# Kernel optimization log

Hardware: AMD Instinct MI355X
Metric: run time of the kernel (lower is better)

## Reference

```python
import jax, jax.numpy as jnp
import numpy as np

D = 1  # dilation


def _unfold3x3(x, d):
    # x: [B, C, H, W] -> [B, H*W, 9, C]; matches torch.nn.Unfold(kernel_size=3,
    # dilation=d, padding=d, stride=1) followed by the module's reshapes.
    B, C, H, W = x.shape
    xp = jnp.pad(x, ((0, 0), (0, 0), (d, d), (d, d)))
    pats = [xp[:, :, i * d:i * d + H, j * d:j * d + W] for i in range(3) for j in range(3)]
    p = jnp.stack(pats, axis=0)  # [9, B, C, H, W], kernel positions row-major (center = 4)
    return p.transpose(1, 3, 4, 0, 2).reshape(B, H * W, 9, C)


def _masked_bn(h, m, gamma, beta, eps=1e-5):
    # BatchNorm1d in training mode applied only to rows selected by bool mask m
    # (the torch code gathers rows, BNs them, scatters back into zeros).
    # Stats are the biased mean/var over the selected rows, per channel.
    axes = tuple(range(h.ndim - 1))
    mf = m[..., None].astype(h.dtype)
    n = jnp.maximum(mf.sum(), 1.0)
    mean = (h * mf).sum(axes) / n
    var = (((h - mean) ** 2 * mf)).sum(axes) / n
    return (h - mean) * jax.lax.rsqrt(var + eps) * gamma + beta


def setup_inputs() -> dict:
    key = jax.random.key(0)
    ks = jax.random.split(key, 8)
    B, H, W = 2, 64, 1024
    Cin, Cout, Cm = 64, 64, 4
    s = 0.1
    x = jax.random.normal(ks[0], (B, Cm + Cin, H, W), jnp.float32)
    mask = (jax.random.uniform(ks[1], (B, 1, H, W)) > 0.3).astype(jnp.float32)
    return {
        "x": x,
        "mask": mask,
        "w1": jax.random.normal(ks[2], (8, Cm), jnp.float32) * s,
        "bn1_g": jnp.ones(8, jnp.float32),
        "bn1_b": jnp.zeros(8, jnp.float32),
        "w2": jax.random.normal(ks[3], (1, 8), jnp.float32) * s,
        "b2": jnp.zeros(1, jnp.float32),
        "g1": jax.random.normal(ks[4], (8, Cm), jnp.float32) * s,
        "gbn1_g": jnp.ones(8, jnp.float32),
        "gbn1_b": jnp.zeros(8, jnp.float32),
        "g2": jax.random.normal(ks[5], (8, 8), jnp.float32) * s,
        "gbn2_g": jnp.ones(8, jnp.float32),
        "gbn2_b": jnp.zeros(8, jnp.float32),
        "w_agg": jax.random.normal(ks[6], (Cout, 72 + Cin), jnp.float32) * s,
        "abn_g": jnp.ones(Cout, jnp.float32),
        "abn_b": jnp.zeros(Cout, jnp.float32),
    }


def reference(x, mask, w1, bn1_g, bn1_b, w2, b2, g1, gbn1_g, gbn1_b, g2, gbn2_g, gbn2_b, w_agg, abn_g, abn_b):
    B, C, H, W = x.shape
    xu = _unfold3x3(x, D)                      # [B, HW, 9, C]
    mu = _unfold3x3(mask, D)[..., 0]           # [B, HW, 9]
    msel = mu > 0                              # valid-neighbor mask
    mp0 = msel[:, :, 4]                        # valid-center mask [B, HW]
    pn = xu[..., :4] - xu[:, :, 4:5, :4]       # relative meta coords [B, HW, 9, 4]
    feats = xu[..., 4:]                        # neighbor features [B, HW, 9, Cin]

    # weight branch (dense compute + mask == torch's gather/scatter)
    h = _masked_bn(pn @ w1.T, msel, bn1_g, bn1_b)
    h = jax.nn.relu(h) @ w2.T + b2             # [B, HW, 9, 1]
    wts = jnp.where(msel, h[..., 0], 0.0)      # zeros at invalid neighbors pre-softmax
    wts = jax.nn.softmax(wts, axis=-1)[..., None]

    fagg = (wts * feats).sum(axis=2)           # [B, HW, Cin]

    # geo branch
    g = jax.nn.relu(_masked_bn(pn @ g1.T, msel, gbn1_g, gbn1_b))
    g = jax.nn.relu(_masked_bn(g @ g2.T, msel, gbn2_g, gbn2_b))
    g = jnp.where(msel[..., None], g, 0.0)
    g = (wts * g).reshape(B, H * W, 72)

    # aggregation over valid centers
    out = jnp.concatenate([fagg, g], axis=-1) @ w_agg.T
    out = jax.nn.relu(_masked_bn(out, mp0, abn_g, abn_b))
    out = jnp.where(mp0[..., None], out, 0.0)  # [B, HW, Cout]
    return out.transpose(0, 2, 1).reshape(B, -1, H, W)  # fold with k=1 == reshape
```

## Files before the change

kernel.cpp:

```cpp
#include <hip/hip_runtime.h>

#define HW_ 65536
#define W_ 1024
#define H_ 64
#define B_ 2
#define C_ 68
#define NPIX 131072
#define EPS 1e-5f
#define SCOLS 258
#define STOT (15 * SCOLS)

typedef __attribute__((ext_vector_type(8))) short short8;
typedef __attribute__((ext_vector_type(4))) float floatx4;

__device__ __forceinline__ unsigned short f2bf(float f) {
  unsigned u = __float_as_uint(f);
  u += 0x7fffu + ((u >> 16) & 1u);
  return (unsigned short)(u >> 16);
}
__device__ __forceinline__ unsigned pack2(float a, float b) {
  return (unsigned)f2bf(a) | ((unsigned)f2bf(b) << 16);
}
__device__ __forceinline__ float wred(float v) {
  v += __shfl_xor(v, 1);  v += __shfl_xor(v, 2);  v += __shfl_xor(v, 4);
  v += __shfl_xor(v, 8);  v += __shfl_xor(v, 16); v += __shfl_xor(v, 32);
  return v;
}
__device__ __forceinline__ int swz_tile(int bid) {
  return (bid & 7) * 64 + (bid >> 3);
}

#define XSTG(ch, row, col) stg[((ch) * 3 + (row)) * SCOLS + (col)]
#define MSTG(row, col)     stg[(12 + (row)) * SCOLS + (col)]

template <int NT>
__device__ __forceinline__ void stage_rows(const float* xb, const float* mb,
                                           int h, int w0, float* stg, int tid) {
#pragma unroll 1
  for (int i = tid; i < STOT; i += NT) {
    int seg = i / SCOLS, col = i - seg * SCOLS;
    int arr = seg / 3, row = seg - arr * 3;
    int wg = w0 - 1 + col, hg = h + row - 1;
    bool ok = ((unsigned)wg < (unsigned)W_) && ((unsigned)hg < (unsigned)H_);
    float v = 0.f;
    if (ok) v = (arr < 4) ? xb[(size_t)arr * HW_ + (hg << 10) + wg]
                          : mb[(hg << 10) + wg];
    stg[i] = v;
  }
}

__global__ __launch_bounds__(256, 4) void k_stats1(
    const float* __restrict__ x, const float* __restrict__ mask,
    const float* __restrict__ w1, const float* __restrict__ g1,
    float* __restrict__ ws) {
  __shared__ float stg[STOT];
  __shared__ float red[4][34];
  int half = blockIdx.x >> 9;
  int tile = swz_tile(blockIdx.x & 511);
  int p0 = tile * 256;
  int b = p0 >> 16, s0 = p0 & (HW_ - 1);
  int h = s0 >> 10, w0 = s0 & (W_ - 1);
  const float* xb = x + (size_t)b * C_ * HW_;
  const float* mb = mask + (size_t)b * HW_;
  stage_rows<256>(xb, mb, h, w0, stg, threadIdx.x);
  __syncthreads();

  int pix = threadIdx.x;
  float xc0 = XSTG(0, 1, 1 + pix), xc1 = XSTG(1, 1, 1 + pix);
  float xc2 = XSTG(2, 1, 1 + pix), xc3 = XSTG(3, 1, 1 + pix);

  float acc[34];
#pragma unroll
  for (int i = 0; i < 34; i++) acc[i] = 0.f;
  if (half == 0) acc[33] = (MSTG(1, 1 + pix) > 0.f) ? 1.f : 0.f;

  int kb = half ? 5 : 0, ke = half ? 9 : 5;
#pragma unroll
  for (int k = 0; k < 9; k++) {
    if (k < kb || k >= ke) continue;
    int row = k / 3, col = 1 + pix + (k % 3 - 1);
    float mval = MSTG(row, col);
    if (mval > 0.f) {
      float pn0 = XSTG(0, row, col) - xc0;
      float pn1 = XSTG(1, row, col) - xc1;
      float pn2 = XSTG(2, row, col) - xc2;
      float pn3 = XSTG(3, row, col) - xc3;
      acc[32] += 1.f;
#pragma unroll
      for (int o = 0; o < 8; o++) {
        float ta = pn0 * w1[o * 4] + pn1 * w1[o * 4 + 1] + pn2 * w1[o * 4 + 2] + pn3 * w1[o * 4 + 3];
        acc[o] += ta; acc[8 + o] += ta * ta;
        float tg = pn0 * g1[o * 4] + pn1 * g1[o * 4 + 1] + pn2 * g1[o * 4 + 2] + pn3 * g1[o * 4 + 3];
        acc[16 + o] += tg; acc[24 + o] += tg * tg;
      }
    }
  }
  int lane = threadIdx.x & 63, wave = threadIdx.x >> 6;
#pragma unroll
  for (int i = 0; i < 34; i++) {
    float rv = wred(acc[i]);
    if (lane == 0) red[wave][i] = rv;
  }
  __syncthreads();
  if (threadIdx.x < 34)
    atomicAdd(&ws[threadIdx.x],
              red[0][threadIdx.x] + red[1][threadIdx.x] + red[2][threadIdx.x] + red[3][threadIdx.x]);
}

__global__ __launch_bounds__(256, 4) void k_stats2(
    const float* __restrict__ x, const float* __restrict__ mask,
    const float* __restrict__ g1, const float* __restrict__ gbn1_g,
    const float* __restrict__ gbn1_b, const float* __restrict__ g2,
    float* __restrict__ ws) {
  __shared__ float stg[STOT];
  __shared__ float red[4][16];
  __shared__ float sc[8], sh[8];
  if (threadIdx.x < 8) {
    int o = threadIdx.x;
    float n = fmaxf(ws[32], 1.f);
    float mean = ws[16 + o] / n;
    float var = ws[24 + o] / n - mean * mean;
    float s_ = gbn1_g[o] * rsqrtf(var + EPS);
    sc[o] = s_; sh[o] = gbn1_b[o] - mean * s_;
  }
  int half = blockIdx.x >> 9;
  int tile = swz_tile(blockIdx.x & 511);
  int p0 = tile * 256;
  int b = p0 >> 16, s0 = p0 & (HW_ - 1);
  int h = s0 >> 10, w0 = s0 & (W_ - 1);
  const float* xb = x + (size_t)b * C_ * HW_;
  const float* mb = mask + (size_t)b * HW_;
  stage_rows<256>(xb, mb, h, w0, stg, threadIdx.x);
  __syncthreads();

  int pix = threadIdx.x;
  float xc0 = XSTG(0, 1, 1 + pix), xc1 = XSTG(1, 1, 1 + pix);
  float xc2 = XSTG(2, 1, 1 + pix), xc3 = XSTG(3, 1, 1 + pix);

  float acc2[16];
#pragma unroll
  for (int i = 0; i < 16; i++) acc2[i] = 0.f;

  int kb = half ? 5 : 0, ke = half ? 9 : 5;
#pragma unroll
  for (int k = 0; k < 9; k++) {
    if (k < kb || k >= ke) continue;
    int row = k / 3, col = 1 + pix + (k % 3 - 1);
    float mval = MSTG(row, col);
    if (mval > 0.f) {
      float pn0 = XSTG(0, row, col) - xc0;
      float pn1 = XSTG(1, row, col) - xc1;
      float pn2 = XSTG(2, row, col) - xc2;
      float pn3 = XSTG(3, row, col) - xc3;
      float gb[8];
#pragma unroll
      for (int o = 0; o < 8; o++) {
        float tg = pn0 * g1[o * 4] + pn1 * g1[o * 4 + 1] + pn2 * g1[o * 4 + 2] + pn3 * g1[o * 4 + 3];
        gb[o] = fmaxf(sc[o] * tg + sh[o], 0.f);
      }
#pragma unroll
      for (int j = 0; j < 8; j++) {
        float t2 = 0.f;
#pragma unroll
        for (int o = 0; o < 8; o++) t2 += gb[o] * g2[j * 8 + o];
        acc2[j] += t2; acc2[8 + j] += t2 * t2;
      }
    }
  }
  int lane = threadIdx.x & 63, wave = threadIdx.x >> 6;
#pragma unroll
  for (int i = 0; i < 16; i++) {
    float rv = wred(acc2[i]);
    if (lane == 0) red[wave][i] = rv;
  }
  __syncthreads();
  if (threadIdx.x < 16)
    atomicAdd(&ws[40 + threadIdx.x],
              red[0][threadIdx.x] + red[1][threadIdx.x] + red[2][threadIdx.x] + red[3][threadIdx.x]);
}

__global__ __launch_bounds__(512, 4) void k_fused(
    const float* __restrict__ x, const float* __restrict__ mask,
    const float* __restrict__ w1, const float* __restrict__ bn1_g,
    const float* __restrict__ bn1_b, const float* __restrict__ w2,
    const float* __restrict__ b2, const float* __restrict__ g1,
    const float* __restrict__ gbn1_g, const float* __restrict__ gbn1_b,
    const float* __restrict__ g2, const float* __restrict__ gbn2_g,
    const float* __restrict__ gbn2_b, const float* __restrict__ w_agg,
    const float* __restrict__ ws, float* __restrict__ out_pre,
    float* __restrict__ wsum) {
  __shared__ uint4 vecA[17][256];
  __shared__ float evb[9][256];
  __shared__ float sA[8], hA[8], sG1[8], hG1[8], sG2[8], hG2[8];
  float* stg = (float*)&vecA[0][0];

  if (threadIdx.x < 24) {
    int o = threadIdx.x & 7;
    float n = fmaxf(ws[32], 1.f);
    float sum, sum2, gma, bta;
    if (threadIdx.x < 8)       { sum = ws[o];      sum2 = ws[8 + o];  gma = bn1_g[o];  bta = bn1_b[o]; }
    else if (threadIdx.x < 16) { sum = ws[16 + o]; sum2 = ws[24 + o]; gma = gbn1_g[o]; bta = gbn1_b[o]; }
    else                       { sum = ws[40 + o]; sum2 = ws[48 + o]; gma = gbn2_g[o]; bta = gbn2_b[o]; }
    float mean = sum / n, var = sum2 / n - mean * mean;
    float s_ = gma * rsqrtf(var + EPS);
    float sft = bta - mean * s_;
    if (threadIdx.x < 8)       { sA[o] = s_;  hA[o] = sft; }
    else if (threadIdx.x < 16) { sG1[o] = s_; hG1[o] = sft; }
    else                       { sG2[o] = s_; hG2[o] = sft; }
  }

  int tid = threadIdx.x;
  int half = tid >> 8;
  int pix = tid & 255;
  int tile = swz_tile(blockIdx.x);
  int p0 = tile * 256;
  int b = p0 >> 16, s0 = p0 & (HW_ - 1);
  int h = s0 >> 10, w0 = s0 & (W_ - 1);
  const float* xb = x + (size_t)b * C_ * HW_;
  const float* mb = mask + (size_t)b * HW_;
  stage_rows<512>(xb, mb, h, w0, stg, tid);
  __syncthreads();

  float xc0 = XSTG(0, 1, 1 + pix), xc1 = XSTG(1, 1, 1 + pix);
  float xc2 = XSTG(2, 1, 1 + pix), xc3 = XSTG(3, 1, 1 + pix);
  float b2v = b2[0];

  float pnc[5][4];
  unsigned mbits = 0u;
  int kb = half ? 5 : 0, ke = half ? 9 : 5;
#pragma unroll
  for (int k = 0; k < 9; k++) {
    if (k < kb || k >= ke) continue;
    int j = k - kb;
    int row = k / 3, col = 1 + pix + (k % 3 - 1);
    float mval = MSTG(row, col);
    float wp = 0.f;
    pnc[j][0] = 0.f; pnc[j][1] = 0.f; pnc[j][2] = 0.f; pnc[j][3] = 0.f;
    if (mval > 0.f) {
      mbits |= (1u << k);
      pnc[j][0] = XSTG(0, row, col) - xc0;
      pnc[j][1] = XSTG(1, row, col) - xc1;
      pnc[j][2] = XSTG(2, row, col) - xc2;
      pnc[j][3] = XSTG(3, row, col) - xc3;
      float accw = 0.f;
#pragma unroll
      for (int o = 0; o < 8; o++) {
        float ta = pnc[j][0] * w1[o * 4] + pnc[j][1] * w1[o * 4 + 1] +
                   pnc[j][2] * w1[o * 4 + 2] + pnc[j][3] * w1[o * 4 + 3];
        accw += fmaxf(sA[o] * ta + hA[o], 0.f) * w2[o];
      }
      wp = accw + b2v;
    }
    evb[k][pix] = wp;
  }
  __syncthreads();

  float ev[9];
  float mx = -1e30f;
#pragma unroll
  for (int k = 0; k < 9; k++) { ev[k] = evb[k][pix]; mx = fmaxf(mx, ev[k]); }
  float den = 0.f;
#pragma unroll
  for (int k = 0; k < 9; k++) { ev[k] = __expf(ev[k] - mx); den += ev[k]; }
  float inv = 1.f / den;

#pragma unroll
  for (int k = 0; k < 9; k++) {
    if (k < kb || k >= ke) continue;
    int j = k - kb;
    uint4 pk; pk.x = pk.y = pk.z = pk.w = 0u;
    if ((mbits >> k) & 1u) {
      float wt = ev[k] * inv;
      float gb[8];
#pragma unroll
      for (int o = 0; o < 8; o++) {
        float tg = pnc[j][0] * g1[o * 4] + pnc[j][1] * g1[o * 4 + 1] +
                   pnc[j][2] * g1[o * 4 + 2] + pnc[j][3] * g1[o * 4 + 3];
        gb[o] = fmaxf(sG1[o] * tg + hG1[o], 0.f);
      }
      float gv[8];
#pragma unroll
      for (int j2 = 0; j2 < 8; j2++) {
        float t2 = 0.f;
#pragma unroll
        for (int o = 0; o < 8; o++) t2 += gb[o] * g2[j2 * 8 + o];
        float gg = fmaxf(sG2[j2] * t2 + hG2[j2], 0.f);
        gv[j2] = wt * gg;
      }
      pk.x = pack2(gv[0], gv[1]); pk.y = pack2(gv[2], gv[3]);
      pk.z = pack2(gv[4], gv[5]); pk.w = pack2(gv[6], gv[7]);
    }
    vecA[8 + k][pix] = pk;
  }

  float facc[32];
#pragma unroll
  for (int c = 0; c < 32; c++) facc[c] = 0.f;
#pragma unroll
  for (int k = 0; k < 9; k++) {
    int di = k / 3 - 1, dj = k % 3 - 1;
    int hh = h + di, ww = w0 + pix + dj;
    bool inb = ((unsigned)hh < (unsigned)H_) && ((unsigned)ww < (unsigned)W_);
    if (inb) {
      int ns = (hh << 10) + ww;
      float wt = ev[k] * inv;
      const float* xf = xb + (size_t)(4 + half * 32) * HW_ + ns;
#pragma unroll
      for (int c = 0; c < 32; c++) facc[c] += wt * xf[(size_t)c * HW_];
    }
  }
#pragma unroll
  for (int c0 = 0; c0 < 32; c0 += 8) {
    uint4 pk;
    pk.x = pack2(facc[c0], facc[c0 + 1]);     pk.y = pack2(facc[c0 + 2], facc[c0 + 3]);
    pk.z = pack2(facc[c0 + 4], facc[c0 + 5]); pk.w = pack2(facc[c0 + 6], facc[c0 + 7]);
    vecA[(half * 32 + c0) >> 3][pix] = pk;
  }
  __syncthreads();

  int lane = tid & 63, wave = tid >> 6;
  int q = lane >> 4, r = lane & 15;
  int wr = wave >> 1, wc = wave & 1;

  short8 Bf[2][5];
#pragma unroll
  for (int nt = 0; nt < 2; nt++) {
    int n = wc * 32 + nt * 16 + r;
#pragma unroll
    for (int ks = 0; ks < 5; ks++) {
      int k0 = ks * 32 + q * 8;
      uint4 pk; pk.x = pk.y = pk.z = pk.w = 0u;
      if (k0 < 136) {
        float4 f0 = *reinterpret_cast<const float4*>(w_agg + n * 136 + k0);
        float4 f1 = *reinterpret_cast<const float4*>(w_agg + n * 136 + k0 + 4);
        pk.x = pack2(f0.x, f0.y); pk.y = pack2(f0.z, f0.w);
        pk.z = pack2(f1.x, f1.y); pk.w = pack2(f1.z, f1.w);
      }
      Bf[nt][ks] = *reinterpret_cast<short8*>(&pk);
    }
  }

  floatx4 acc[4][2];
#pragma unroll
  for (int m = 0; m < 4; m++)
#pragma unroll
    for (int nt = 0; nt < 2; nt++) acc[m][nt] = (floatx4){0.f, 0.f, 0.f, 0.f};

#pragma unroll
  for (int m = 0; m < 4; m++) {
    int pixm = (wr * 4 + m) * 16 + r;
    short8 Af[5];
#pragma unroll
    for (int ks = 0; ks < 5; ks++) {
      int chunk = ks * 4 + q;
      if (chunk < 17)
        Af[ks] = *reinterpret_cast<const short8*>(&vecA[chunk][pixm]);
      else
        Af[ks] = (short8){0, 0, 0, 0, 0, 0, 0, 0};
    }
#pragma unroll
    for (int nt = 0; nt < 2; nt++)
#pragma unroll
      for (int ks = 0; ks < 5; ks++)
        acc[m][nt] = __builtin_amdgcn_mfma_f32_16x16x32_bf16(Af[ks], Bf[nt][ks], acc[m][nt], 0, 0, 0);
  }

  float aS[2] = {0.f, 0.f}, aQ[2] = {0.f, 0.f};
#pragma unroll
  for (int m = 0; m < 4; m++) {
    int mt = wr * 4 + m;
    int srow = s0 + mt * 16 + q * 4;
    float4 mv = *reinterpret_cast<const float4*>(mb + srow);
    float m0 = (mv.x > 0.f) ? 1.f : 0.f, m1 = (mv.y > 0.f) ? 1.f : 0.f;
    float m2 = (mv.z > 0.f) ? 1.f : 0.f, m3 = (mv.w > 0.f) ? 1.f : 0.f;
#pragma unroll
    for (int nt = 0; nt < 2; nt++) {
      int ch = wc * 32 + nt * 16 + r;
      float4 ov;
      ov.x = acc[m][nt][0]; ov.y = acc[m][nt][1];
      ov.z = acc[m][nt][2]; ov.w = acc[m][nt][3];
      aS[nt] += ov.x * m0 + ov.y * m1 + ov.z * m2 + ov.w * m3;
      aQ[nt] += ov.x * ov.x * m0 + ov.y * ov.y * m1 + ov.z * ov.z * m2 + ov.w * ov.w * m3;
      *reinterpret_cast<float4*>(out_pre + ((size_t)(b * 64 + ch)) * HW_ + srow) = ov;
    }
  }

  __syncthreads();
  float* rS = (float*)&vecA[0][0];
  float* rQ = rS + 256;
#pragma unroll
  for (int nt = 0; nt < 2; nt++) {
    float v1 = aS[nt], v2 = aQ[nt];
    v1 += __shfl_xor(v1, 16); v1 += __shfl_xor(v1, 32);
    v2 += __shfl_xor(v2, 16); v2 += __shfl_xor(v2, 32);
    if (lane < 16) { rS[wave * 32 + nt * 16 + lane] = v1; rQ[wave * 32 + nt * 16 + lane] = v2; }
  }
  __syncthreads();
  if (tid < 64) {
    int c = tid;
    int wc_ = c >> 5, nt_ = (c >> 4) & 1, r_ = c & 15;
    float s1 = 0.f, s2 = 0.f;
#pragma unroll
    for (int wr_ = 0; wr_ < 4; wr_++) {
      int idx = (wr_ * 2 + wc_) * 32 + nt_ * 16 + r_;
      s1 += rS[idx]; s2 += rQ[idx];
    }
    atomicAdd(&wsum[64 + c], s1);
    atomicAdd(&wsum[128 + c], s2);
  }
}

__global__ __launch_bounds__(256) void k_final(
    const float* __restrict__ out_pre, const float* __restrict__ mask,
    const float* __restrict__ abn_g, const float* __restrict__ abn_b,
    const float* __restrict__ ws, float* __restrict__ out) {
  __shared__ float sc[64], sh[64];
  if (threadIdx.x < 64) {
    int c = threadIdx.x;
    float n0 = fmaxf(ws[33], 1.f);
    float mean = ws[64 + c] / n0;
    float var = ws[128 + c] / n0 - mean * mean;
    float s_ = abn_g[c] * rsqrtf(var + EPS);
    sc[c] = s_; sh[c] = abn_b[c] - mean * s_;
  }
  __syncthreads();
  int i4 = (blockIdx.x * 256 + threadIdx.x) * 4;
  if (i4 >= B_ * 64 * HW_) return;
  int c = (i4 >> 16) & 63;
  int b = i4 >> 22;
  int s = i4 & (HW_ - 1);
  float4 v = *reinterpret_cast<const float4*>(out_pre + i4);
  float4 m = *reinterpret_cast<const float4*>(mask + (size_t)b * HW_ + s);
  float4 o;
  o.x = (m.x > 0.f) ? fmaxf(v.x * sc[c] + sh[c], 0.f) : 0.f;
  o.y = (m.y > 0.f) ? fmaxf(v.y * sc[c] + sh[c], 0.f) : 0.f;
  o.z = (m.z > 0.f) ? fmaxf(v.z * sc[c] + sh[c], 0.f) : 0.f;
  o.w = (m.w > 0.f) ? fmaxf(v.w * sc[c] + sh[c], 0.f) : 0.f;
  *reinterpret_cast<float4*>(out + i4) = o;
}

extern "C" void kernel_launch(void* const* d_in, const int* in_sizes, int n_in,
                              void* d_out, int out_size, void* d_ws, size_t ws_size,
                              hipStream_t stream) {
  const float* x      = (const float*)d_in[0];
  const float* mask   = (const float*)d_in[1];
  const float* w1     = (const float*)d_in[2];
  const float* bn1_g  = (const float*)d_in[3];
  const float* bn1_b  = (const float*)d_in[4];
  const float* w2     = (const float*)d_in[5];
  const float* b2     = (const float*)d_in[6];
  const float* g1     = (const float*)d_in[7];
  const float* gbn1_g = (const float*)d_in[8];
  const float* gbn1_b = (const float*)d_in[9];
  const float* g2     = (const float*)d_in[10];
  const float* gbn2_g = (const float*)d_in[11];
  const float* gbn2_b = (const float*)d_in[12];
  const float* w_agg  = (const float*)d_in[13];
  const float* abn_g  = (const float*)d_in[14];
  const float* abn_b  = (const float*)d_in[15];
  float* out = (float*)d_out;

  size_t need = 1024 + (size_t)NPIX * 64 * 4;
  if (ws_size < need) return;

  float* wsf = (float*)d_ws;
  float* out_pre = (float*)((char*)d_ws + 1024);

  hipMemsetAsync(d_ws, 0, 1024, stream);
  k_stats1<<<1024, 256, 0, stream>>>(x, mask, w1, g1, wsf);
  k_stats2<<<1024, 256, 0, stream>>>(x, mask, g1, gbn1_g, gbn1_b, g2, wsf);
  k_fused<<<512, 512, 0, stream>>>(x, mask, w1, bn1_g, bn1_b, w2, b2, g1,
                                   gbn1_g, gbn1_b, g2, gbn2_g, gbn2_b, w_agg,
                                   wsf, out_pre, wsf);
  k_final<<<8192, 256, 0, stream>>>(out_pre, mask, abn_g, abn_b, wsf, out);
}
```

Before: 209.9 us.

## Use moment statistics for linear BN layers and store pre-BN output as bf16

The first stats kernel now accumulates raw first and second moments of the relative coordinates (4 sums plus 10 cross products) instead of per-channel sums for both 8-channel projections. The BN mean and variance for w1 and g1 are then rebuilt analytically in later kernels, which halves the stats1 grid and its FMA work. Separately, the intermediate pre-BN aggregation output is written as bf16 and read back in the final kernel, halving that round-trip traffic. The cost is lost precision in the stored intermediate and possible cancellation error in the moment-based variance.

```diff
diff --git a/kernel.cpp b/kernel.cpp
--- a/kernel.cpp
+++ b/kernel.cpp
@@ -20,6 +20,9 @@
 }
 __device__ __forceinline__ unsigned pack2(float a, float b) {
   return (unsigned)f2bf(a) | ((unsigned)f2bf(b) << 16);
+}
+__device__ __forceinline__ float bf2f(unsigned u) {
+  return __uint_as_float(u << 16);
 }
 __device__ __forceinline__ float wred(float v) {
   v += __shfl_xor(v, 1);  v += __shfl_xor(v, 2);  v += __shfl_xor(v, 4);
@@ -51,12 +54,10 @@
 
 __global__ __launch_bounds__(256, 4) void k_stats1(
     const float* __restrict__ x, const float* __restrict__ mask,
-    const float* __restrict__ w1, const float* __restrict__ g1,
     float* __restrict__ ws) {
   __shared__ float stg[STOT];
-  __shared__ float red[4][34];
-  int half = blockIdx.x >> 9;
-  int tile = swz_tile(blockIdx.x & 511);
+  __shared__ float red[4][16];
+  int tile = swz_tile(blockIdx.x);
   int p0 = tile * 256;
   int b = p0 >> 16, s0 = p0 & (HW_ - 1);
   int h = s0 >> 10, w0 = s0 & (W_ - 1);
@@ -69,15 +70,13 @@
   float xc0 = XSTG(0, 1, 1 + pix), xc1 = XSTG(1, 1, 1 + pix);
   float xc2 = XSTG(2, 1, 1 + pix), xc3 = XSTG(3, 1, 1 + pix);
 
-  float acc[34];
-#pragma unroll
-  for (int i = 0; i < 34; i++) acc[i] = 0.f;
-  if (half == 0) acc[33] = (MSTG(1, 1 + pix) > 0.f) ? 1.f : 0.f;
-
-  int kb = half ? 5 : 0, ke = half ? 9 : 5;
+  float a[16];
+#pragma unroll
+  for (int i = 0; i < 16; i++) a[i] = 0.f;
+  a[15] = (MSTG(1, 1 + pix) > 0.f) ? 1.f : 0.f;
+
 #pragma unroll
   for (int k = 0; k < 9; k++) {
-    if (k < kb || k >= ke) continue;
     int row = k / 3, col = 1 + pix + (k % 3 - 1);
     float mval = MSTG(row, col);
     if (mval > 0.f) {
@@ -85,24 +84,21 @@
       float pn1 = XSTG(1, row, col) - xc1;
       float pn2 = XSTG(2, row, col) - xc2;
       float pn3 = XSTG(3, row, col) - xc3;
-      acc[32] += 1.f;
-#pragma unroll
-      for (int o = 0; o < 8; o++) {
-        float ta = pn0 * w1[o * 4] + pn1 * w1[o * 4 + 1] + pn2 * w1[o * 4 + 2] + pn3 * w1[o * 4 + 3];
-        acc[o] += ta; acc[8 + o] += ta * ta;
-        float tg = pn0 * g1[o * 4] + pn1 * g1[o * 4 + 1] + pn2 * g1[o * 4 + 2] + pn3 * g1[o * 4 + 3];
-        acc[16 + o] += tg; acc[24 + o] += tg * tg;
-      }
+      a[14] += 1.f;
+      a[0] += pn0; a[1] += pn1; a[2] += pn2; a[3] += pn3;
+      a[4] += pn0 * pn0; a[5] += pn0 * pn1; a[6] += pn0 * pn2; a[7] += pn0 * pn3;
+      a[8] += pn1 * pn1; a[9] += pn1 * pn2; a[10] += pn1 * pn3;
+      a[11] += pn2 * pn2; a[12] += pn2 * pn3; a[13] += pn3 * pn3;
     }
   }
   int lane = threadIdx.x & 63, wave = threadIdx.x >> 6;
 #pragma unroll
-  for (int i = 0; i < 34; i++) {
-    float rv = wred(acc[i]);
+  for (int i = 0; i < 16; i++) {
+    float rv = wred(a[i]);
     if (lane == 0) red[wave][i] = rv;
   }
   __syncthreads();
-  if (threadIdx.x < 34)
+  if (threadIdx.x < 16)
     atomicAdd(&ws[threadIdx.x],
               red[0][threadIdx.x] + red[1][threadIdx.x] + red[2][threadIdx.x] + red[3][threadIdx.x]);
 }
@@ -117,9 +113,13 @@
   __shared__ float sc[8], sh[8];
   if (threadIdx.x < 8) {
     int o = threadIdx.x;
-    float n = fmaxf(ws[32], 1.f);
-    float mean = ws[16 + o] / n;
-    float var = ws[24 + o] / n - mean * mean;
+    float a0 = g1[o * 4], a1 = g1[o * 4 + 1], a2 = g1[o * 4 + 2], a3 = g1[o * 4 + 3];
+    float n = fmaxf(ws[14], 1.f);
+    float mean = (a0 * ws[0] + a1 * ws[1] + a2 * ws[2] + a3 * ws[3]) / n;
+    float q = a0 * a0 * ws[4] + a1 * a1 * ws[8] + a2 * a2 * ws[11] + a3 * a3 * ws[13]
+            + 2.f * (a0 * a1 * ws[5] + a0 * a2 * ws[6] + a0 * a3 * ws[7]
+                   + a1 * a2 * ws[9] + a1 * a3 * ws[10] + a2 * a3 * ws[12]);
+    float var = q / n - mean * mean;
     float s_ = gbn1_g[o] * rsqrtf(var + EPS);
     sc[o] = s_; sh[o] = gbn1_b[o] - mean * s_;
   }
@@ -187,26 +187,35 @@
     const float* __restrict__ gbn1_g, const float* __restrict__ gbn1_b,
     const float* __restrict__ g2, const float* __restrict__ gbn2_g,
     const float* __restrict__ gbn2_b, const float* __restrict__ w_agg,
-    const float* __restrict__ ws, float* __restrict__ out_pre,
+    const float* __restrict__ ws, unsigned short* __restrict__ out_pre,
     float* __restrict__ wsum) {
   __shared__ uint4 vecA[17][256];
   __shared__ float evb[9][256];
   __shared__ float sA[8], hA[8], sG1[8], hG1[8], sG2[8], hG2[8];
   float* stg = (float*)&vecA[0][0];
 
-  if (threadIdx.x < 24) {
+  if (threadIdx.x < 16) {
     int o = threadIdx.x & 7;
-    float n = fmaxf(ws[32], 1.f);
-    float sum, sum2, gma, bta;
-    if (threadIdx.x < 8)       { sum = ws[o];      sum2 = ws[8 + o];  gma = bn1_g[o];  bta = bn1_b[o]; }
-    else if (threadIdx.x < 16) { sum = ws[16 + o]; sum2 = ws[24 + o]; gma = gbn1_g[o]; bta = gbn1_b[o]; }
-    else                       { sum = ws[40 + o]; sum2 = ws[48 + o]; gma = gbn2_g[o]; bta = gbn2_b[o]; }
-    float mean = sum / n, var = sum2 / n - mean * mean;
+    const float* wv = (threadIdx.x < 8) ? w1 : g1;
+    float a0 = wv[o * 4], a1 = wv[o * 4 + 1], a2 = wv[o * 4 + 2], a3 = wv[o * 4 + 3];
+    float n = fmaxf(ws[14], 1.f);
+    float mean = (a0 * ws[0] + a1 * ws[1] + a2 * ws[2] + a3 * ws[3]) / n;
+    float q = a0 * a0 * ws[4] + a1 * a1 * ws[8] + a2 * a2 * ws[11] + a3 * a3 * ws[13]
+            + 2.f * (a0 * a1 * ws[5] + a0 * a2 * ws[6] + a0 * a3 * ws[7]
+                   + a1 * a2 * ws[9] + a1 * a3 * ws[10] + a2 * a3 * ws[12]);
+    float var = q / n - mean * mean;
+    float gma = (threadIdx.x < 8) ? bn1_g[o] : gbn1_g[o];
+    float bta = (threadIdx.x < 8) ? bn1_b[o] : gbn1_b[o];
     float s_ = gma * rsqrtf(var + EPS);
     float sft = bta - mean * s_;
-    if (threadIdx.x < 8)       { sA[o] = s_;  hA[o] = sft; }
-    else if (threadIdx.x < 16) { sG1[o] = s_; hG1[o] = sft; }
-    else                       { sG2[o] = s_; hG2[o] = sft; }
+    if (threadIdx.x < 8) { sA[o] = s_;  hA[o] = sft; }
+    else                 { sG1[o] = s_; hG1[o] = sft; }
+  } else if (threadIdx.x < 24) {
+    int o = threadIdx.x & 7;
+    float n = fmaxf(ws[14], 1.f);
+    float mean = ws[40 + o] / n, var = ws[48 + o] / n - mean * mean;
+    float s_ = gbn2_g[o] * rsqrtf(var + EPS);
+    sG2[o] = s_; hG2[o] = gbn2_b[o] - mean * s_;
   }
 
   int tid = threadIdx.x;
@@ -376,12 +385,13 @@
 #pragma unroll
     for (int nt = 0; nt < 2; nt++) {
       int ch = wc * 32 + nt * 16 + r;
-      float4 ov;
-      ov.x = acc[m][nt][0]; ov.y = acc[m][nt][1];
-      ov.z = acc[m][nt][2]; ov.w = acc[m][nt][3];
-      aS[nt] += ov.x * m0 + ov.y * m1 + ov.z * m2 + ov.w * m3;
-      aQ[nt] += ov.x * ov.x * m0 + ov.y * ov.y * m1 + ov.z * ov.z * m2 + ov.w * ov.w * m3;
-      *reinterpret_cast<float4*>(out_pre + ((size_t)(b * 64 + ch)) * HW_ + srow) = ov;
+      aS[nt] += acc[m][nt][0] * m0 + acc[m][nt][1] * m1 + acc[m][nt][2] * m2 + acc[m][nt][3] * m3;
+      aQ[nt] += acc[m][nt][0] * acc[m][nt][0] * m0 + acc[m][nt][1] * acc[m][nt][1] * m1 +
+                acc[m][nt][2] * acc[m][nt][2] * m2 + acc[m][nt][3] * acc[m][nt][3] * m3;
+      uint2 st;
+      st.x = pack2(acc[m][nt][0], acc[m][nt][1]);
+      st.y = pack2(acc[m][nt][2], acc[m][nt][3]);
+      *reinterpret_cast<uint2*>(out_pre + ((size_t)(b * 64 + ch)) * HW_ + srow) = st;
     }
   }
 
@@ -411,32 +421,39 @@
 }
 
 __global__ __launch_bounds__(256) void k_final(
-    const float* __restrict__ out_pre, const float* __restrict__ mask,
+    const unsigned short* __restrict__ out_pre, const float* __restrict__ mask,
     const float* __restrict__ abn_g, const float* __restrict__ abn_b,
     const float* __restrict__ ws, float* __restrict__ out) {
   __shared__ float sc[64], sh[64];
   if (threadIdx.x < 64) {
     int c = threadIdx.x;
-    float n0 = fmaxf(ws[33], 1.f);
+    float n0 = fmaxf(ws[15], 1.f);
     float mean = ws[64 + c] / n0;
     float var = ws[128 + c] / n0 - mean * mean;
     float s_ = abn_g[c] * rsqrtf(var + EPS);
     sc[c] = s_; sh[c] = abn_b[c] - mean * s_;
   }
   __syncthreads();
-  int i4 = (blockIdx.x * 256 + threadIdx.x) * 4;
-  if (i4 >= B_ * 64 * HW_) return;
-  int c = (i4 >> 16) & 63;
-  int b = i4 >> 22;
-  int s = i4 & (HW_ - 1);
-  float4 v = *reinterpret_cast<const float4*>(out_pre + i4);
-  float4 m = *reinterpret_cast<const float4*>(mask + (size_t)b * HW_ + s);
-  float4 o;
-  o.x = (m.x > 0.f) ? fmaxf(v.x * sc[c] + sh[c], 0.f) : 0.f;
-  o.y = (m.y > 0.f) ? fmaxf(v.y * sc[c] + sh[c], 0.f) : 0.f;
-  o.z = (m.z > 0.f) ? fmaxf(v.z * sc[c] + sh[c], 0.f) : 0.f;
-  o.w = (m.w > 0.f) ? fmaxf(v.w * sc[c] + sh[c], 0.f) : 0.f;
-  *reinterpret_cast<float4*>(out + i4) = o;
+  int i8 = (blockIdx.x * 256 + threadIdx.x) * 8;
+  if (i8 >= B_ * 64 * HW_) return;
+  int c = (i8 >> 16) & 63;
+  int b = i8 >> 22;
+  int s = i8 & (HW_ - 1);
+  uint4 v = *reinterpret_cast<const uint4*>(out_pre + i8);
+  float4 m0 = *reinterpret_cast<const float4*>(mask + (size_t)b * HW_ + s);
+  float4 m1 = *reinterpret_cast<const float4*>(mask + (size_t)b * HW_ + s + 4);
+  float scv = sc[c], shv = sh[c];
+  float4 o0, o1;
+  o0.x = (m0.x > 0.f) ? fmaxf(bf2f(v.x & 0xffffu) * scv + shv, 0.f) : 0.f;
+  o0.y = (m0.y > 0.f) ? fmaxf(bf2f(v.x >> 16) * scv + shv, 0.f) : 0.f;
+  o0.z = (m0.z > 0.f) ? fmaxf(bf2f(v.y & 0xffffu) * scv + shv, 0.f) : 0.f;
+  o0.w = (m0.w > 0.f) ? fmaxf(bf2f(v.y >> 16) * scv + shv, 0.f) : 0.f;
+  o1.x = (m1.x > 0.f) ? fmaxf(bf2f(v.z & 0xffffu) * scv + shv, 0.f) : 0.f;
+  o1.y = (m1.y > 0.f) ? fmaxf(bf2f(v.z >> 16) * scv + shv, 0.f) : 0.f;
+  o1.z = (m1.z > 0.f) ? fmaxf(bf2f(v.w & 0xffffu) * scv + shv, 0.f) : 0.f;
+  o1.w = (m1.w > 0.f) ? fmaxf(bf2f(v.w >> 16) * scv + shv, 0.f) : 0.f;
+  *reinterpret_cast<float4*>(out + i8) = o0;
+  *reinterpret_cast<float4*>(out + i8 + 4) = o1;
 }
 
 extern "C" void kernel_launch(void* const* d_in, const int* in_sizes, int n_in,
@@ -460,17 +477,17 @@
   const float* abn_b  = (const float*)d_in[15];
   float* out = (float*)d_out;
 
-  size_t need = 1024 + (size_t)NPIX * 64 * 4;
+  size_t need = 1024 + (size_t)NPIX * 64 * 2;
   if (ws_size < need) return;
 
   float* wsf = (float*)d_ws;
-  float* out_pre = (float*)((char*)d_ws + 1024);
+  unsigned short* out_pre = (unsigned short*)((char*)d_ws + 1024);
 
   hipMemsetAsync(d_ws, 0, 1024, stream);
-  k_stats1<<<1024, 256, 0, stream>>>(x, mask, w1, g1, wsf);
+  k_stats1<<<512, 256, 0, stream>>>(x, mask, wsf);
   k_stats2<<<1024, 256, 0, stream>>>(x, mask, g1, gbn1_g, gbn1_b, g2, wsf);
   k_fused<<<512, 512, 0, stream>>>(x, mask, w1, bn1_g, bn1_b, w2, b2, g1,
                                    gbn1_g, gbn1_b, g2, gbn2_g, gbn2_b, w_agg,
                                    wsf, out_pre, wsf);
-  k_final<<<8192, 256, 0, stream>>>(out_pre, mask, abn_g, abn_b, wsf, out);
-}
+  k_final<<<4096, 256, 0, stream>>>(out_pre, mask, abn_g, abn_b, wsf, out);
+}
```

Result: faster. 190.1 us (-9.4%).
